# Kernel tuning notes

Hardware: AMD Instinct MI355X
Metric: run time of the kernel (lower is better)

Reference implementation:

```python
import jax, jax.numpy as jnp
import numpy as np

C, R = 256, 16
H = C // R  # 16


def setup_inputs() -> dict:
    key = jax.random.key(0)
    ks = jax.random.split(key, 16)
    s = lambda k, shape, scale: jax.random.normal(k, shape, dtype=jnp.float32) * scale
    return {
        "x": jax.random.normal(ks[0], (16, C, 128, 128), dtype=jnp.float32),
        # SE block for std descriptor
        "sw1": s(ks[1], (H, C), 1.0 / np.sqrt(C)),
        "sb1": jnp.zeros((H,), jnp.float32),
        "sw2": s(ks[2], (C, H), 1.0 / np.sqrt(H)),
        "sb2": jnp.zeros((C,), jnp.float32),
        # SE block for mean descriptor
        "mw1": s(ks[3], (H, C), 1.0 / np.sqrt(C)),
        "mb1": jnp.zeros((H,), jnp.float32),
        "mw2": s(ks[4], (C, H), 1.0 / np.sqrt(H)),
        "mb2": jnp.zeros((C,), jnp.float32),
        # bottleneck 2C -> C
        "bw": s(ks[5], (C, 2 * C), 1.0 / np.sqrt(2 * C)),
        "bb": jnp.zeros((C,), jnp.float32),
        # final SE block
        "fw1": s(ks[6], (H, C), 1.0 / np.sqrt(C)),
        "fb1": jnp.zeros((H,), jnp.float32),
        "fw2": s(ks[7], (C, H), 1.0 / np.sqrt(H)),
        "fb2": jnp.zeros((C,), jnp.float32),
    }


def _se(d, w1, b1, w2, b2):
    # d: [B, C]; 1x1 convs on [B,C,1,1] == dense matmuls on channel dim
    h = jax.nn.relu(jnp.einsum("bc,hc->bh", d, w1) + b1)
    return jnp.einsum("bh,ch->bc", h, w2) + b2


def reference(x, sw1, sb1, sw2, sb2, mw1, mb1, mw2, mb2, bw, bb, fw1, fb1, fw2, fb2):
    # channel descriptors: spatial mean and (biased) std per (batch, channel)
    mean = jnp.mean(x, axis=(2, 3))  # [B, C]
    var = jnp.mean((x - mean[:, :, None, None]) ** 2, axis=(2, 3))
    std = jnp.sqrt(var)

    ref_std = _se(std, sw1, sb1, sw2, sb2)
    ref_mean = _se(mean, mw1, mb1, mw2, mb2)

    fused = jnp.concatenate([ref_std, ref_mean], axis=1)  # [B, 2C]
    fused = jax.nn.relu(jnp.einsum("bd,cd->bc", fused, bw) + bb)  # bottleneck
    fused = _se(fused, fw1, fb1, fw2, fb2)

    mask = jax.nn.sigmoid(fused)  # [B, C]
    return x * mask[:, :, None, None]
```

## Files before the change

kernel.cpp:

```cpp
#include <hip/hip_runtime.h>
#include <hip/hip_bf16.h>
#include <math.h>

#define BATCH 16
#define CH    256
#define HID   16
#define SPAT  16384

typedef float vfloat4 __attribute__((ext_vector_type(4)));

__global__ __launch_bounds__(256) void stats_kernel(const float* __restrict__ x,
                                                    float* __restrict__ mean_g,
                                                    float* __restrict__ std_g)
{
    const long long base = (long long)blockIdx.x * SPAT;
    const vfloat4* x4 = reinterpret_cast<const vfloat4*>(x + base);

    float s = 0.f, s2 = 0.f;
    #pragma unroll
    for (int i = 0; i < 16; ++i) {
        vfloat4 v = x4[threadIdx.x + i * 256];
        s  += v.x + v.y + v.z + v.w;
        s2 += v.x * v.x + v.y * v.y + v.z * v.z + v.w * v.w;
    }

    #pragma unroll
    for (int off = 32; off > 0; off >>= 1) {
        s  += __shfl_xor(s,  off);
        s2 += __shfl_xor(s2, off);
    }

    __shared__ float ws[4], ws2[4];
    const int wave = threadIdx.x >> 6;
    const int lane = threadIdx.x & 63;
    if (lane == 0) { ws[wave] = s; ws2[wave] = s2; }
    __syncthreads();

    if (threadIdx.x == 0) {
        const float ts  = ws[0]  + ws[1]  + ws[2]  + ws[3];
        const float ts2 = ws2[0] + ws2[1] + ws2[2] + ws2[3];
        const float m   = ts * (1.f / SPAT);
        const float var = ts2 * (1.f / SPAT) - m * m;
        mean_g[blockIdx.x] = m;
        std_g[blockIdx.x]  = sqrtf(fmaxf(var, 0.f));
    }
}

__global__ __launch_bounds__(256) void se_chain_kernel(
    const float* __restrict__ mean_g, const float* __restrict__ std_g,
    const float* __restrict__ sw1, const float* __restrict__ sb1,
    const float* __restrict__ sw2, const float* __restrict__ sb2,
    const float* __restrict__ mw1, const float* __restrict__ mb1,
    const float* __restrict__ mw2, const float* __restrict__ mb2,
    const float* __restrict__ bw,  const float* __restrict__ bb,
    const float* __restrict__ fw1, const float* __restrict__ fb1,
    const float* __restrict__ fw2, const float* __restrict__ fb2,
    float* __restrict__ mask_g)
{
    const int b   = blockIdx.x;
    const int tid = threadIdx.x;

    __shared__ float s_desc[2 * CH];
    __shared__ float s_h[HID];
    __shared__ float s_fused[2 * CH];
    __shared__ float s_g[CH];

    s_desc[tid]      = std_g [b * CH + tid];
    s_desc[CH + tid] = mean_g[b * CH + tid];
    __syncthreads();

    auto se_l1 = [&](const float* desc, const float* __restrict__ w1,
                     const float* __restrict__ b1) {
        const int hh = tid >> 4;
        const int j  = tid & 15;
        float acc = 0.f;
        #pragma unroll
        for (int k = 0; k < 16; ++k) {
            const int c = j * 16 + k;
            acc += desc[c] * w1[hh * CH + c];
        }
        #pragma unroll
        for (int off = 1; off < 16; off <<= 1)
            acc += __shfl_xor(acc, off, 16);
        if (j == 0) s_h[hh] = fmaxf(acc + b1[hh], 0.f);
    };

    auto se_l2 = [&](const float* __restrict__ w2, const float* __restrict__ b2,
                     float* outbuf) {
        float acc = b2[tid];
        const vfloat4* w4 = reinterpret_cast<const vfloat4*>(w2 + tid * HID);
        #pragma unroll
        for (int q = 0; q < 4; ++q) {
            const vfloat4 w = w4[q];
            acc += s_h[q * 4 + 0] * w.x + s_h[q * 4 + 1] * w.y
                 + s_h[q * 4 + 2] * w.z + s_h[q * 4 + 3] * w.w;
        }
        outbuf[tid] = acc;
    };

    se_l1(s_desc, sw1, sb1);
    __syncthreads();
    se_l2(sw2, sb2, s_fused);
    __syncthreads();

    se_l1(s_desc + CH, mw1, mb1);
    __syncthreads();
    se_l2(mw2, mb2, s_fused + CH);
    __syncthreads();

    {
        float acc = bb[tid];
        const vfloat4* wrow = reinterpret_cast<const vfloat4*>(bw + tid * (2 * CH));
        const vfloat4* f4   = reinterpret_cast<const vfloat4*>(s_fused);
        #pragma unroll 8
        for (int q = 0; q < (2 * CH) / 4; ++q) {
            const vfloat4 w = wrow[q];
            const vfloat4 f = f4[q];
            acc += f.x * w.x + f.y * w.y + f.z * w.z + f.w * w.w;
        }
        s_g[tid] = fmaxf(acc, 0.f);
    }
    __syncthreads();

    se_l1(s_g, fw1, fb1);
    __syncthreads();
    {
        float acc = fb2[tid];
        const vfloat4* w4 = reinterpret_cast<const vfloat4*>(fw2 + tid * HID);
        #pragma unroll
        for (int q = 0; q < 4; ++q) {
            const vfloat4 w = w4[q];
            acc += s_h[q * 4 + 0] * w.x + s_h[q * 4 + 1] * w.y
                 + s_h[q * 4 + 2] * w.z + s_h[q * 4 + 3] * w.w;
        }
        mask_g[b * CH + tid] = 1.f / (1.f + expf(-acc));
    }
}

__global__ __launch_bounds__(256) void scale_kernel(const float* __restrict__ x,
                                                    const float* __restrict__ mask,
                                                    float* __restrict__ out)
{
    const int plane = (BATCH * CH - 1) - blockIdx.x;
    const float m = mask[plane];
    const long long base = (long long)plane * SPAT;
    const vfloat4* x4 = reinterpret_cast<const vfloat4*>(x + base);
    vfloat4*       o4 = reinterpret_cast<vfloat4*>(out + base);
    #pragma unroll
    for (int i = 0; i < 16; ++i) {
        vfloat4 v = x4[threadIdx.x + i * 256];
        v *= m;
        __builtin_nontemporal_store(v, &o4[threadIdx.x + i * 256]);
    }
}

extern "C" void kernel_launch(void* const* d_in, const int* in_sizes, int n_in,
                              void* d_out, int out_size, void* d_ws, size_t ws_size,
                              hipStream_t stream)
{
    const float* x   = (const float*)d_in[0];
    const float* sw1 = (const float*)d_in[1];
    const float* sb1 = (const float*)d_in[2];
    const float* sw2 = (const float*)d_in[3];
    const float* sb2 = (const float*)d_in[4];
    const float* mw1 = (const float*)d_in[5];
    const float* mb1 = (const float*)d_in[6];
    const float* mw2 = (const float*)d_in[7];
    const float* mb2 = (const float*)d_in[8];
    const float* bw  = (const float*)d_in[9];
    const float* bb  = (const float*)d_in[10];
    const float* fw1 = (const float*)d_in[11];
    const float* fb1 = (const float*)d_in[12];
    const float* fw2 = (const float*)d_in[13];
    const float* fb2 = (const float*)d_in[14];

    float* out = (float*)d_out;

    float* ws     = (float*)d_ws;
    float* mean_g = ws;
    float* std_g  = ws + BATCH * CH;
    float* mask_g = ws + 2 * BATCH * CH;

    const int nbc = BATCH * CH;

    stats_kernel<<<nbc, 256, 0, stream>>>(x, mean_g, std_g);
    se_chain_kernel<<<BATCH, 256, 0, stream>>>(mean_g, std_g,
                                               sw1, sb1, sw2, sb2,
                                               mw1, mb1, mw2, mb2,
                                               bw, bb,
                                               fw1, fb1, fw2, fb2,
                                               mask_g);
    scale_kernel<<<nbc, 256, 0, stream>>>(x, mask_g, out);
}
```

Baseline: 148.4 us.

## Fuse SE chain into scale kernel, recomputing the mask per plane block

Drops the separate single-batch-row SE chain kernel and the mask buffer. Each scale block now recomputes the full SE/bottleneck chain for its batch row, keeps the one channel's sigmoid in shared memory, then scales the plane. This removes one kernel launch and the serialization gap between stages. The cost is 4096-fold redundant work, mainly re-reading the 256x512 bottleneck weights through cache in every block, ahead of the streaming scale.

```diff
diff --git a/kernel.cpp b/kernel.cpp
--- a/kernel.cpp
+++ b/kernel.cpp
@@ -6,6 +6,7 @@
 #define CH    256
 #define HID   16
 #define SPAT  16384
+#define NPLANE (BATCH * CH)
 
 typedef float vfloat4 __attribute__((ext_vector_type(4)));
 
@@ -46,7 +47,8 @@
     }
 }
 
-__global__ __launch_bounds__(256) void se_chain_kernel(
+__global__ __launch_bounds__(256) void scale_fused_kernel(
+    const float* __restrict__ x,
     const float* __restrict__ mean_g, const float* __restrict__ std_g,
     const float* __restrict__ sw1, const float* __restrict__ sb1,
     const float* __restrict__ sw2, const float* __restrict__ sb2,
@@ -55,18 +57,21 @@
     const float* __restrict__ bw,  const float* __restrict__ bb,
     const float* __restrict__ fw1, const float* __restrict__ fb1,
     const float* __restrict__ fw2, const float* __restrict__ fb2,
-    float* __restrict__ mask_g)
+    float* __restrict__ out)
 {
-    const int b   = blockIdx.x;
-    const int tid = threadIdx.x;
+    const int plane = (NPLANE - 1) - blockIdx.x;
+    const int brow  = plane >> 8;
+    const int mych  = plane & 255;
+    const int tid   = threadIdx.x;
 
     __shared__ float s_desc[2 * CH];
     __shared__ float s_h[HID];
     __shared__ float s_fused[2 * CH];
     __shared__ float s_g[CH];
+    __shared__ float s_mval;
 
-    s_desc[tid]      = std_g [b * CH + tid];
-    s_desc[CH + tid] = mean_g[b * CH + tid];
+    s_desc[tid]      = std_g [brow * CH + tid];
+    s_desc[CH + tid] = mean_g[brow * CH + tid];
     __syncthreads();
 
     auto se_l1 = [&](const float* desc, const float* __restrict__ w1,
@@ -84,16 +89,15 @@
             acc += __shfl_xor(acc, off, 16);
         if (j == 0) s_h[hh] = fmaxf(acc + b1[hh], 0.f);
     };
-
     auto se_l2 = [&](const float* __restrict__ w2, const float* __restrict__ b2,
                      float* outbuf) {
         float acc = b2[tid];
         const vfloat4* w4 = reinterpret_cast<const vfloat4*>(w2 + tid * HID);
         #pragma unroll
         for (int q = 0; q < 4; ++q) {
-            const vfloat4 w = w4[q];
-            acc += s_h[q * 4 + 0] * w.x + s_h[q * 4 + 1] * w.y
-                 + s_h[q * 4 + 2] * w.z + s_h[q * 4 + 3] * w.w;
+            const vfloat4 wv = w4[q];
+            acc += s_h[q * 4 + 0] * wv.x + s_h[q * 4 + 1] * wv.y
+                 + s_h[q * 4 + 2] * wv.z + s_h[q * 4 + 3] * wv.w;
         }
         outbuf[tid] = acc;
     };
@@ -102,7 +106,6 @@
     __syncthreads();
     se_l2(sw2, sb2, s_fused);
     __syncthreads();
-
     se_l1(s_desc + CH, mw1, mb1);
     __syncthreads();
     se_l2(mw2, mb2, s_fused + CH);
@@ -114,9 +117,9 @@
         const vfloat4* f4   = reinterpret_cast<const vfloat4*>(s_fused);
         #pragma unroll 8
         for (int q = 0; q < (2 * CH) / 4; ++q) {
-            const vfloat4 w = wrow[q];
-            const vfloat4 f = f4[q];
-            acc += f.x * w.x + f.y * w.y + f.z * w.z + f.w * w.w;
+            const vfloat4 wv = wrow[q];
+            const vfloat4 fv = f4[q];
+            acc += fv.x * wv.x + fv.y * wv.y + fv.z * wv.z + fv.w * wv.w;
         }
         s_g[tid] = fmaxf(acc, 0.f);
     }
@@ -129,28 +132,24 @@
         const vfloat4* w4 = reinterpret_cast<const vfloat4*>(fw2 + tid * HID);
         #pragma unroll
         for (int q = 0; q < 4; ++q) {
-            const vfloat4 w = w4[q];
-            acc += s_h[q * 4 + 0] * w.x + s_h[q * 4 + 1] * w.y
-                 + s_h[q * 4 + 2] * w.z + s_h[q * 4 + 3] * w.w;
+            const vfloat4 wv = w4[q];
+            acc += s_h[q * 4 + 0] * wv.x + s_h[q * 4 + 1] * wv.y
+                 + s_h[q * 4 + 2] * wv.z + s_h[q * 4 + 3] * wv.w;
         }
-        mask_g[b * CH + tid] = 1.f / (1.f + expf(-acc));
+        if (tid == mych)
+            s_mval = 1.f / (1.f + expf(-acc));
     }
-}
+    __syncthreads();
 
-__global__ __launch_bounds__(256) void scale_kernel(const float* __restrict__ x,
-                                                    const float* __restrict__ mask,
-                                                    float* __restrict__ out)
-{
-    const int plane = (BATCH * CH - 1) - blockIdx.x;
-    const float m = mask[plane];
+    const float m = s_mval;
     const long long base = (long long)plane * SPAT;
     const vfloat4* x4 = reinterpret_cast<const vfloat4*>(x + base);
     vfloat4*       o4 = reinterpret_cast<vfloat4*>(out + base);
     #pragma unroll
     for (int i = 0; i < 16; ++i) {
-        vfloat4 v = x4[threadIdx.x + i * 256];
+        vfloat4 v = x4[tid + i * 256];
         v *= m;
-        __builtin_nontemporal_store(v, &o4[threadIdx.x + i * 256]);
+        __builtin_nontemporal_store(v, &o4[tid + i * 256]);
     }
 }
 
@@ -176,19 +175,14 @@
 
     float* out = (float*)d_out;
 
-    float* ws     = (float*)d_ws;
-    float* mean_g = ws;
-    float* std_g  = ws + BATCH * CH;
-    float* mask_g = ws + 2 * BATCH * CH;
+    float* mean_g = (float*)d_ws;
+    float* std_g  = mean_g + NPLANE;
 
-    const int nbc = BATCH * CH;
-
-    stats_kernel<<<nbc, 256, 0, stream>>>(x, mean_g, std_g);
-    se_chain_kernel<<<BATCH, 256, 0, stream>>>(mean_g, std_g,
-                                               sw1, sb1, sw2, sb2,
-                                               mw1, mb1, mw2, mb2,
-                                               bw, bb,
-                                               fw1, fb1, fw2, fb2,
-                                               mask_g);
-    scale_kernel<<<nbc, 256, 0, stream>>>(x, mask_g, out);
+    stats_kernel<<<NPLANE, 256, 0, stream>>>(x, mean_g, std_g);
+    scale_fused_kernel<<<NPLANE, 256, 0, stream>>>(x, mean_g, std_g,
+                                                   sw1, sb1, sw2, sb2,
+                                                   mw1, mb1, mw2, mb2,
+                                                   bw, bb,
+                                                   fw1, fb1, fw2, fb2,
+                                                   out);
 }
```

Result: slower. 314.8 us (+112.1%).
